# Kernel optimization log

Measured on AMD Instinct MI355X. Metric: run time of the kernel, lower is better.

The kernel has to match this reference:

```python
import jax, jax.numpy as jnp
import numpy as np

D = 256; H = 4; DK = 32; DV = D // H; DFF = 1024
NTF = 600; NG = 8000
EPS = 1e-5


def layer_norm(x, g, b):
    m = jnp.mean(x, -1, keepdims=True)
    v = jnp.mean((x - m) ** 2, -1, keepdims=True)
    return (x - m) / jnp.sqrt(v + EPS) * g + b


def setup_inputs() -> dict:
    key = jax.random.key(0)
    ks = jax.random.split(key, 32)
    def nrm(i, shape, s=1.0):
        return jax.random.normal(ks[i], shape, dtype=jnp.float32) * s
    w = 0.02  # init scale for weights
    inp = {
        "H_TF": nrm(0, (NTF, D)),
        "H_G": nrm(1, (NG, D)),
        "z_exp": nrm(2, (NG, D)),
        "z_seq": nrm(3, (NG, D)),
        "z_txt": nrm(4, (NG, D)),
        "tf_idx": jax.random.randint(ks[5], (NTF,), 0, NG),
        "WQ_seq": nrm(6, (H * DK, D), w), "WK_seq": nrm(7, (H * DK, D), w),
        "WQ_exp": nrm(8, (H * DK, D), w), "WK_exp": nrm(9, (H * DK, D), w),
        "WQ_txt": nrm(10, (H * DK, D), w), "WK_txt": nrm(11, (H * DK, D), w),
        "gate_w": jnp.broadcast_to(jnp.eye(3, dtype=jnp.float32), (H, 3, 3)),
        "gate_b": jnp.zeros((H, 3), jnp.float32),
        "WVG": nrm(12, (D, D), w), "WVTF": nrm(13, (D, D), w),
        "WOTF": nrm(14, (D, D), w), "WOG": nrm(15, (D, D), w),
        "ln_atf_g": jnp.ones((D,), jnp.float32), "ln_atf_b": jnp.zeros((D,), jnp.float32),
        "ln_ag_g": jnp.ones((D,), jnp.float32), "ln_ag_b": jnp.zeros((D,), jnp.float32),
        "ln_ftf_g": jnp.ones((D,), jnp.float32), "ln_ftf_b": jnp.zeros((D,), jnp.float32),
        "ln_fg_g": jnp.ones((D,), jnp.float32), "ln_fg_b": jnp.zeros((D,), jnp.float32),
        "ftf_W1": nrm(16, (DFF, D), w), "ftf_b1": jnp.zeros((DFF,), jnp.float32),
        "ftf_W2": nrm(17, (D, DFF), w), "ftf_b2": jnp.zeros((D,), jnp.float32),
        "fg_W1": nrm(18, (DFF, D), w), "fg_b1": jnp.zeros((DFF,), jnp.float32),
        "fg_W2": nrm(19, (D, DFF), w), "fg_b2": jnp.zeros((D,), jnp.float32),
    }
    return inp


def reference(H_TF, H_G, z_exp, z_seq, z_txt, tf_idx,
              WQ_seq, WK_seq, WQ_exp, WK_exp, WQ_txt, WK_txt,
              gate_w, gate_b, WVG, WVTF, WOTF, WOG,
              ln_atf_g, ln_atf_b, ln_ag_g, ln_ag_b,
              ln_ftf_g, ln_ftf_b, ln_fg_g, ln_fg_b,
              ftf_W1, ftf_b1, ftf_W2, ftf_b2,
              fg_W1, fg_b1, fg_W2, fg_b2):
    n_tf, n_gene = H_TF.shape[0], H_G.shape[0]
    scale = float(DK) ** 0.5

    H_TF_n = layer_norm(H_TF, ln_atf_g, ln_atf_b)
    H_G_n = layer_norm(H_G, ln_ag_g, ln_ag_b)

    z_seq_tf = z_seq[tf_idx]; z_exp_tf = z_exp[tf_idx]; z_txt_tf = z_txt[tf_idx]
    Q_seq = (z_seq_tf @ WQ_seq.T).reshape(n_tf, H, DK)
    K_seq = (z_seq @ WK_seq.T).reshape(n_gene, H, DK)
    Q_exp = (z_exp_tf @ WQ_exp.T).reshape(n_tf, H, DK)
    K_exp = (z_exp @ WK_exp.T).reshape(n_gene, H, DK)
    Q_txt = (z_txt_tf @ WQ_txt.T).reshape(n_tf, H, DK)
    K_txt = (z_txt @ WK_txt.T).reshape(n_gene, H, DK)

    s_bind = jnp.einsum('thd,ghd->htg', Q_seq, K_seq) / scale
    s_coexpr = jnp.einsum('thd,ghd->htg', Q_exp, K_exp) / scale
    s_know = jnp.einsum('thd,ghd->htg', Q_txt, K_txt) / scale

    # evidence gate: per-(head,tf,gene) softmax mixture over the 3 evidence channels
    s = jnp.stack([s_bind, s_coexpr, s_know], axis=-1)            # [H, t, g, 3]
    logits = jnp.einsum('htge,hef->htgf', s, gate_w) + gate_b[:, None, None, :]
    alpha = jax.nn.softmax(logits, axis=-1)                        # [H, t, g, 3]
    u = jnp.einsum('htge,htge->htg', alpha, s)                     # gated mixture
    A = jax.nn.softmax(u, axis=-1)                                 # softmax over genes

    V_G = (H_G_n @ WVG.T).reshape(n_gene, H, DV)
    V_TF = (H_TF_n @ WVTF.T).reshape(n_tf, H, DV)
    out_tf = jnp.einsum('htg,ghv->thv', A, V_G).reshape(n_tf, D) @ WOTF.T
    out_g = jnp.einsum('htg,thv->ghv', A, V_TF).reshape(n_gene, D) @ WOG.T

    H_TF2 = H_TF + out_tf
    H_G2 = H_G + out_g

    x = layer_norm(H_TF2, ln_ftf_g, ln_ftf_b)
    H_TF3 = H_TF2 + jax.nn.gelu(x @ ftf_W1.T + ftf_b1, approximate=False) @ ftf_W2.T + ftf_b2
    y = layer_norm(H_G2, ln_fg_g, ln_fg_b)
    H_G3 = H_G2 + jax.nn.gelu(y @ fg_W1.T + fg_b1, approximate=False) @ fg_W2.T + fg_b2

    return (H_TF3, H_G3, A.mean(0), u.mean(0), alpha.mean(0))
```

## Files before the change

### kernel.cpp

```cpp
#include <hip/hip_runtime.h>
#include <hip/hip_bf16.h>

#define NTF 600
#define NG  8000
#define DD  256
#define HH  4
#define DKK 32
#define DVV 64
#define DFF 1024

typedef __attribute__((ext_vector_type(8))) short frag_ab;
typedef __attribute__((ext_vector_type(4))) float frag_cd;

__device__ __forceinline__ unsigned short f2bu(float f) {
    __hip_bfloat16 h = __float2bfloat16(f);
    return __builtin_bit_cast(unsigned short, h);
}
__device__ __forceinline__ short f2bs(float f) { return (short)f2bu(f); }

__global__ __launch_bounds__(256)
void cvt3_kernel(const float* __restrict__ a, const float* __restrict__ b, const float* __restrict__ c,
                 unsigned short* __restrict__ oa, unsigned short* __restrict__ ob,
                 unsigned short* __restrict__ oc, int n4) {
    for (int i = blockIdx.x * 256 + threadIdx.x; i < 3 * n4; i += gridDim.x * 256) {
        int sel = i / n4, j = i - sel * n4;
        const float* src = (sel == 0) ? a : (sel == 1) ? b : c;
        unsigned short* dst = (sel == 0) ? oa : (sel == 1) ? ob : oc;
        float4 v = ((const float4*)src)[j];
        ushort4 o = {f2bu(v.x), f2bu(v.y), f2bu(v.z), f2bu(v.w)};
        ((ushort4*)dst)[j] = o;
    }
}

__global__ __launch_bounds__(256)
void cvt_w_kernel(const float* s0, const float* s1, const float* s2, const float* s3,
                  const float* s4, const float* s5, const float* s6, const float* s7,
                  const float* s8, const float* s9, const float* s10, const float* s11,
                  const float* s12, unsigned short* __restrict__ dst) {
    const int y = blockIdx.y;
    const float* src; int off, n;
    switch (y) {
        case 0:  src = s0;  off = 0;       n = 32768;  break;
        case 1:  src = s1;  off = 32768;   n = 32768;  break;
        case 2:  src = s2;  off = 65536;   n = 32768;  break;
        case 3:  src = s3;  off = 98304;   n = 32768;  break;
        case 4:  src = s4;  off = 131072;  n = 32768;  break;
        case 5:  src = s5;  off = 163840;  n = 32768;  break;
        case 6:  src = s6;  off = 196608;  n = 65536;  break;
        case 7:  src = s7;  off = 262144;  n = 65536;  break;
        case 8:  src = s8;  off = 327680;  n = 65536;  break;
        case 9:  src = s9;  off = 393216;  n = 262144; break;
        case 10: src = s10; off = 655360;  n = 262144; break;
        case 11: src = s11; off = 917504;  n = 262144; break;
        default: src = s12; off = 1179648; n = 262144; break;
    }
    const int n4 = n >> 2;
    for (int i = blockIdx.x * 256 + threadIdx.x; i < n4; i += gridDim.x * 256) {
        float4 v = ((const float4*)src)[i];
        ushort4 o = {f2bu(v.x), f2bu(v.y), f2bu(v.z), f2bu(v.w)};
        ((ushort4*)(dst + off))[i] = o;
    }
}

__global__ __launch_bounds__(64)
void ln_b_kernel(const float* __restrict__ x, const float* __restrict__ g,
                 const float* __restrict__ b, unsigned short* __restrict__ y) {
    int row = blockIdx.x;
    int tid = threadIdx.x;
    const float4* xp = (const float4*)(x + (size_t)row * DD);
    float4 v = xp[tid];
    float s = v.x + v.y + v.z + v.w;
    #pragma unroll
    for (int off = 32; off > 0; off >>= 1) s += __shfl_xor(s, off, 64);
    float mean = s * (1.f / 256.f);
    float dx = v.x - mean, dy = v.y - mean, dz = v.z - mean, dw = v.w - mean;
    float q = dx*dx + dy*dy + dz*dz + dw*dw;
    #pragma unroll
    for (int off = 32; off > 0; off >>= 1) q += __shfl_xor(q, off, 64);
    float inv = rsqrtf(q * (1.f / 256.f) + 1e-5f);
    float4 gg = ((const float4*)g)[tid];
    float4 bb = ((const float4*)b)[tid];
    ushort4 o = {f2bu(dx * inv * gg.x + bb.x), f2bu(dy * inv * gg.y + bb.y),
                 f2bu(dz * inv * gg.z + bb.z), f2bu(dw * inv * gg.w + bb.w)};
    ((ushort4*)(y + (size_t)row * DD))[tid] = o;
}

__global__ __launch_bounds__(256)
void gather_b_kernel(const float* __restrict__ zs, const float* __restrict__ ze,
                     const float* __restrict__ zt, const int* __restrict__ idx,
                     unsigned short* __restrict__ os, unsigned short* __restrict__ oe,
                     unsigned short* __restrict__ ot) {
    int t = blockIdx.x, j = threadIdx.x;
    size_t src = (size_t)idx[t] * DD + j;
    size_t dst = (size_t)t * DD + j;
    os[dst] = f2bu(zs[src]);
    oe[dst] = f2bu(ze[src]);
    ot[dst] = f2bu(zt[src]);
}

template<bool XF32, bool BIAS, bool GELU, bool RES, bool OB16>
__device__ __forceinline__
void mgemm_core(const void* __restrict__ Xv, const unsigned short* __restrict__ W,
                const float* __restrict__ bias, const float* __restrict__ res,
                void* __restrict__ Yv, int M, int N, int K) {
    const int lane = threadIdx.x & 63, wv = threadIdx.x >> 6;
    const int wm = wv >> 1, wn = wv & 1;
    const int lr = lane & 15, lk = lane >> 4;
    const int m0 = blockIdx.x * 64, n0 = blockIdx.y * 128;
    frag_cd zz = {0.f, 0.f, 0.f, 0.f};
    frag_cd acc[2][4];
    #pragma unroll
    for (int mi = 0; mi < 2; ++mi)
        #pragma unroll
        for (int ni = 0; ni < 4; ++ni) acc[mi][ni] = zz;
    int arow[2], brow[4];
    #pragma unroll
    for (int mi = 0; mi < 2; ++mi) arow[mi] = min(m0 + wm * 32 + mi * 16 + lr, M - 1);
    #pragma unroll
    for (int ni = 0; ni < 4; ++ni) brow[ni] = n0 + wn * 64 + ni * 16 + lr;
    for (int k0 = 0; k0 < K; k0 += 32) {
        frag_ab af[2], bfr[4];
        #pragma unroll
        for (int mi = 0; mi < 2; ++mi) {
            if (XF32) {
                const float* xp = (const float*)Xv + (size_t)arow[mi] * K + k0 + lk * 8;
                float4 v0 = *(const float4*)xp;
                float4 v1 = *(const float4*)(xp + 4);
                frag_ab t;
                t[0] = f2bs(v0.x); t[1] = f2bs(v0.y); t[2] = f2bs(v0.z); t[3] = f2bs(v0.w);
                t[4] = f2bs(v1.x); t[5] = f2bs(v1.y); t[6] = f2bs(v1.z); t[7] = f2bs(v1.w);
                af[mi] = t;
            } else {
                af[mi] = *(const frag_ab*)((const unsigned short*)Xv + (size_t)arow[mi] * K + k0 + lk * 8);
            }
        }
        #pragma unroll
        for (int ni = 0; ni < 4; ++ni)
            bfr[ni] = *(const frag_ab*)(W + (size_t)brow[ni] * K + k0 + lk * 8);
        #pragma unroll
        for (int mi = 0; mi < 2; ++mi)
            #pragma unroll
            for (int ni = 0; ni < 4; ++ni)
                acc[mi][ni] = __builtin_amdgcn_mfma_f32_16x16x32_bf16(af[mi], bfr[ni], acc[mi][ni], 0, 0, 0);
    }
    #pragma unroll
    for (int ni = 0; ni < 4; ++ni) {
        const int n = brow[ni];
        const float bn = BIAS ? bias[n] : 0.f;
        #pragma unroll
        for (int mi = 0; mi < 2; ++mi) {
            #pragma unroll
            for (int r = 0; r < 4; ++r) {
                const int m = m0 + wm * 32 + mi * 16 + lk * 4 + r;
                if (m < M) {
                    float v = acc[mi][ni][r] + bn;
                    if (GELU) v = 0.5f * v * (1.f + erff(v * 0.70710678118654752f));
                    if (RES)  v += res[(size_t)m * N + n];
                    if (OB16) ((unsigned short*)Yv)[(size_t)m * N + n] = f2bu(v);
                    else      ((float*)Yv)[(size_t)m * N + n] = v;
                }
            }
        }
    }
}

template<bool XF32, bool BIAS, bool GELU, bool RES, bool OB16>
__global__ __launch_bounds__(256)
void mgemm_kernel(const void* __restrict__ X, const unsigned short* __restrict__ W,
                  const float* __restrict__ bias, const float* __restrict__ res,
                  void* __restrict__ Y, int M, int N, int K) {
    mgemm_core<XF32, BIAS, GELU, RES, OB16>(X, W, bias, res, Y, M, N, K);
}

__global__ __launch_bounds__(256)
void mgemm3_kernel(const unsigned short* X0, const unsigned short* W0, unsigned short* Y0,
                   const unsigned short* X1, const unsigned short* W1, unsigned short* Y1,
                   const unsigned short* X2, const unsigned short* W2, unsigned short* Y2,
                   int M, int N, int K) {
    const unsigned short* X = (blockIdx.z == 0) ? X0 : (blockIdx.z == 1) ? X1 : X2;
    const unsigned short* W = (blockIdx.z == 0) ? W0 : (blockIdx.z == 1) ? W1 : W2;
    unsigned short*       Y = (blockIdx.z == 0) ? Y0 : (blockIdx.z == 1) ? Y1 : Y2;
    mgemm_core<false, false, false, false, true>(X, W, nullptr, nullptr, Y, M, N, K);
}

__global__ __launch_bounds__(256)
void scores_mfma(const unsigned short* __restrict__ Qse, const unsigned short* __restrict__ Qex,
                 const unsigned short* __restrict__ Qtx,
                 const unsigned short* __restrict__ Kse, const unsigned short* __restrict__ Kex,
                 const unsigned short* __restrict__ Ktx,
                 const float* __restrict__ gw, const float* __restrict__ gb,
                 float* __restrict__ U, float* __restrict__ umean, float* __restrict__ amean) {
    const int lane = threadIdx.x & 63, wv = threadIdx.x >> 6;
    const int lr = lane & 15, lk = lane >> 4;
    const int t0 = blockIdx.x * 64 + wv * 16;
    const int g0 = blockIdx.y * 64;
    const int tq = min(t0 + lr, NTF - 1);
    frag_cd zz = {0.f, 0.f, 0.f, 0.f};

    frag_ab qf[3][4];
    #pragma unroll
    for (int h = 0; h < HH; ++h) {
        qf[0][h] = *(const frag_ab*)(Qse + (size_t)tq * 128 + h * DKK + lk * 8);
        qf[1][h] = *(const frag_ab*)(Qex + (size_t)tq * 128 + h * DKK + lk * 8);
        qf[2][h] = *(const frag_ab*)(Qtx + (size_t)tq * 128 + h * DKK + lk * 8);
    }
    float gwr[HH][3][3], gbr[HH][3];
    #pragma unroll
    for (int h = 0; h < HH; ++h) {
        #pragma unroll
        for (int e = 0; e < 3; ++e)
            #pragma unroll
            for (int f = 0; f < 3; ++f) gwr[h][e][f] = gw[h * 9 + e * 3 + f];
        #pragma unroll
        for (int f = 0; f < 3; ++f) gbr[h][f] = gb[h * 3 + f];
    }
    const float sc = 0.17677669529663687f;

    #pragma unroll
    for (int gi = 0; gi < 4; ++gi) {
        const int gg = g0 + gi * 16;
        const int gk = gg + lr;
        float us[4] = {0.f, 0.f, 0.f, 0.f};
        float a0s[4] = {0.f, 0.f, 0.f, 0.f};
        float a1s[4] = {0.f, 0.f, 0.f, 0.f};
        float a2s[4] = {0.f, 0.f, 0.f, 0.f};
        #pragma unroll
        for (int h = 0; h < HH; ++h) {
            frag_ab kf0 = *(const frag_ab*)(Kse + (size_t)gk * 128 + h * DKK + lk * 8);
            frag_ab kf1 = *(const frag_ab*)(Kex + (size_t)gk * 128 + h * DKK + lk * 8);
            frag_ab kf2 = *(const frag_ab*)(Ktx + (size_t)gk * 128 + h * DKK + lk * 8);
            frag_cd s0 = __builtin_amdgcn_mfma_f32_16x16x32_bf16(qf[0][h], kf0, zz, 0, 0, 0);
            frag_cd s1 = __builtin_amdgcn_mfma_f32_16x16x32_bf16(qf[1][h], kf1, zz, 0, 0, 0);
            frag_cd s2 = __builtin_amdgcn_mfma_f32_16x16x32_bf16(qf[2][h], kf2, zz, 0, 0, 0);
            #pragma unroll
            for (int r = 0; r < 4; ++r) {
                const int t = t0 + lk * 4 + r;
                float e0 = s0[r] * sc, e1 = s1[r] * sc, e2 = s2[r] * sc;
                float lg0 = e0 * gwr[h][0][0] + e1 * gwr[h][1][0] + e2 * gwr[h][2][0] + gbr[h][0];
                float lg1 = e0 * gwr[h][0][1] + e1 * gwr[h][1][1] + e2 * gwr[h][2][1] + gbr[h][1];
                float lg2 = e0 * gwr[h][0][2] + e1 * gwr[h][1][2] + e2 * gwr[h][2][2] + gbr[h][2];
                float mx = fmaxf(lg0, fmaxf(lg1, lg2));
                float x0 = __expf(lg0 - mx), x1 = __expf(lg1 - mx), x2 = __expf(lg2 - mx);
                float inv = 1.f / (x0 + x1 + x2);
                float a0 = x0 * inv, a1 = x1 * inv, a2 = x2 * inv;
                float u = a0 * e0 + a1 * e1 + a2 * e2;
                if (t < NTF) U[((size_t)h * NTF + t) * NG + gg + lr] = u;
                us[r] += u; a0s[r] += a0; a1s[r] += a1; a2s[r] += a2;
            }
        }
        #pragma unroll
        for (int r = 0; r < 4; ++r) {
            const int t = t0 + lk * 4 + r;
            if (t < NTF) {
                size_t p = (size_t)t * NG + gg + lr;
                umean[p] = us[r] * 0.25f;
                amean[p * 3 + 0] = a0s[r] * 0.25f;
                amean[p * 3 + 1] = a1s[r] * 0.25f;
                amean[p * 3 + 2] = a2s[r] * 0.25f;
            }
        }
    }
}

__global__ __launch_bounds__(512)
void softmax_amean_kernel(float* __restrict__ U, float* __restrict__ Am) {
    __shared__ float sred[8];
    const int t = blockIdx.x, tid = threadIdx.x;
    const int w = tid >> 6;
    float am[16] = {};
    for (int h = 0; h < HH; ++h) {
        float* p = U + ((size_t)h * NTF + t) * NG;
        float v[16];
        float mx = -1e30f;
        #pragma unroll
        for (int i = 0; i < 16; ++i) {
            int j = i * 512 + tid;
            v[i] = (j < NG) ? p[j] : -1e30f;
            mx = fmaxf(mx, v[i]);
        }
        #pragma unroll
        for (int off = 32; off > 0; off >>= 1) mx = fmaxf(mx, __shfl_xor(mx, off, 64));
        __syncthreads();
        if ((tid & 63) == 0) sred[w] = mx;
        __syncthreads();
        mx = sred[0];
        #pragma unroll
        for (int k = 1; k < 8; ++k) mx = fmaxf(mx, sred[k]);
        float sum = 0.f;
        #pragma unroll
        for (int i = 0; i < 16; ++i) {
            int j = i * 512 + tid;
            v[i] = (j < NG) ? __expf(v[i] - mx) : 0.f;
            sum += v[i];
        }
        #pragma unroll
        for (int off = 32; off > 0; off >>= 1) sum += __shfl_xor(sum, off, 64);
        __syncthreads();
        if ((tid & 63) == 0) sred[w] = sum;
        __syncthreads();
        float tot = 0.f;
        #pragma unroll
        for (int k = 0; k < 8; ++k) tot += sred[k];
        float inv = 1.f / tot;
        #pragma unroll
        for (int i = 0; i < 16; ++i) {
            int j = i * 512 + tid;
            float a = v[i] * inv;
            if (j < NG) p[j] = a;
            am[i] += a;
        }
    }
    #pragma unroll
    for (int i = 0; i < 16; ++i) {
        int j = i * 512 + tid;
        if (j < NG) Am[(size_t)t * NG + j] = am[i] * 0.25f;
    }
}

__global__ __launch_bounds__(256)
void attn_tf_kernel(const float* __restrict__ A, const float* __restrict__ VG,
                    float* __restrict__ AT) {
    __shared__ float As[16][68];
    __shared__ float Vs[16][68];
    const int tid = threadIdx.x;
    const int tx = tid & 15, ty = tid >> 4;
    const int m0 = blockIdx.x * 64;
    const int h  = blockIdx.y;
    const int g0 = blockIdx.z * 512;
    const float* Ah = A + (size_t)h * NTF * NG;
    float acc[4][4] = {};
    for (int kk = 0; kk < 512; kk += 16) {
        __syncthreads();
        #pragma unroll
        for (int j = 0; j < 4; ++j) {
            int idx = j * 256 + tid;
            int k = idx & 15, m = idx >> 4;
            int t = m0 + m, g = g0 + kk + k;
            As[k][m] = (t < NTF && g < NG) ? Ah[(size_t)t * NG + g] : 0.f;
            int v = idx & 63, k2 = idx >> 6;
            int g2 = g0 + kk + k2;
            Vs[k2][v] = (g2 < NG) ? VG[(size_t)g2 * DD + h * DVV + v] : 0.f;
        }
        __syncthreads();
        #pragma unroll
        for (int k = 0; k < 16; ++k) {
            float4 a4 = *(const float4*)&As[k][ty * 4];
            float4 b4 = *(const float4*)&Vs[k][tx * 4];
            float a[4] = {a4.x, a4.y, a4.z, a4.w};
            float b[4] = {b4.x, b4.y, b4.z, b4.w};
            #pragma unroll
            for (int i = 0; i < 4; ++i)
                #pragma unroll
                for (int j = 0; j < 4; ++j)
                    acc[i][j] += a[i] * b[j];
        }
    }
    #pragma unroll
    for (int i = 0; i < 4; ++i) {
        int t = m0 + ty * 4 + i;
        if (t >= NTF) continue;
        #pragma unroll
        for (int j = 0; j < 4; ++j)
            atomicAdd(&AT[(size_t)t * DD + h * DVV + tx * 4 + j], acc[i][j]);
    }
}

__global__ __launch_bounds__(256)
void attn_g_kernel(const float* __restrict__ A, const float* __restrict__ VTF,
                   unsigned short* __restrict__ ATb) {
    __shared__ float As[16][68];
    __shared__ float Vs[16][68];
    const int tid = threadIdx.x;
    const int tx = tid & 15, ty = tid >> 4;
    const int g0 = blockIdx.x * 64;
    const int h  = blockIdx.y;
    const float* Ah = A + (size_t)h * NTF * NG;
    float acc[4][4] = {};
    for (int t0 = 0; t0 < NTF; t0 += 16) {
        __syncthreads();
        #pragma unroll
        for (int j = 0; j < 4; ++j) {
            int idx = j * 256 + tid;
            int m = idx & 63, k = idx >> 6;
            int t = t0 + k;
            As[k][m] = (t < NTF) ? Ah[(size_t)t * NG + g0 + m] : 0.f;
            Vs[k][m] = (t < NTF) ? VTF[(size_t)t * DD + h * DVV + m] : 0.f;
        }
        __syncthreads();
        #pragma unroll
        for (int k = 0; k < 16; ++k) {
            float4 a4 = *(const float4*)&As[k][ty * 4];
            float4 b4 = *(const float4*)&Vs[k][tx * 4];
            float a[4] = {a4.x, a4.y, a4.z, a4.w};
            float b[4] = {b4.x, b4.y, b4.z, b4.w};
            #pragma unroll
            for (int i = 0; i < 4; ++i)
                #pragma unroll
                for (int j = 0; j < 4; ++j)
                    acc[i][j] += a[i] * b[j];
        }
    }
    #pragma unroll
    for (int i = 0; i < 4; ++i) {
        ushort4 o = {f2bu(acc[i][0]), f2bu(acc[i][1]), f2bu(acc[i][2]), f2bu(acc[i][3])};
        *(ushort4*)&ATb[(size_t)(g0 + ty * 4 + i) * DD + h * DVV + tx * 4] = o;
    }
}

template<bool RES>
__global__ __launch_bounds__(256)
void gemm_xwt(const float* __restrict__ X, const float* __restrict__ W,
              const float* __restrict__ res, float* __restrict__ Y, int M, int N, int K) {
    __shared__ float Xs[16][132];
    __shared__ float Ws[16][132];
    const int tid = threadIdx.x;
    const int bm = blockIdx.x * 128, bn = blockIdx.y * 128;
    const int tx = tid & 15, ty = tid >> 4;
    float acc[8][8] = {};
    for (int k0 = 0; k0 < K; k0 += 16) {
        __syncthreads();
        #pragma unroll
        for (int j = 0; j < 8; ++j) {
            int idx = j * 256 + tid;
            int k = idx & 15, m = idx >> 4;
            Xs[k][m] = (bm + m < M) ? X[(size_t)(bm + m) * K + k0 + k] : 0.f;
            Ws[k][m] = W[(size_t)(bn + m) * K + k0 + k];
        }
        __syncthreads();
        #pragma unroll
        for (int k = 0; k < 16; ++k) {
            float4 a0 = *(const float4*)&Xs[k][ty * 8];
            float4 a1 = *(const float4*)&Xs[k][ty * 8 + 4];
            float4 b0 = *(const float4*)&Ws[k][tx * 8];
            float4 b1 = *(const float4*)&Ws[k][tx * 8 + 4];
            float a[8] = {a0.x,a0.y,a0.z,a0.w,a1.x,a1.y,a1.z,a1.w};
            float b[8] = {b0.x,b0.y,b0.z,b0.w,b1.x,b1.y,b1.z,b1.w};
            #pragma unroll
            for (int i = 0; i < 8; ++i)
                #pragma unroll
                for (int j = 0; j < 8; ++j)
                    acc[i][j] += a[i] * b[j];
        }
    }
    #pragma unroll
    for (int i = 0; i < 8; ++i) {
        int m = bm + ty * 8 + i;
        if (m >= M) continue;
        #pragma unroll
        for (int j = 0; j < 8; ++j) {
            int n = bn + tx * 8 + j;
            float v = acc[i][j];
            if (RES) v += res[(size_t)m * N + n];
            Y[(size_t)m * N + n] = v;
        }
    }
}

extern "C" void kernel_launch(void* const* d_in, const int* in_sizes, int n_in,
                              void* d_out, int out_size, void* d_ws, size_t ws_size,
                              hipStream_t stream) {
    (void)in_sizes; (void)n_in; (void)out_size; (void)ws_size;
    const float* H_TF   = (const float*)d_in[0];
    const float* H_G    = (const float*)d_in[1];
    const float* z_exp  = (const float*)d_in[2];
    const float* z_seq  = (const float*)d_in[3];
    const float* z_txt  = (const float*)d_in[4];
    const int*   tf_idx = (const int*)d_in[5];
    const float* WQ_seq = (const float*)d_in[6];
    const float* WK_seq = (const float*)d_in[7];
    const float* WQ_exp = (const float*)d_in[8];
    const float* WK_exp = (const float*)d_in[9];
    const float* WQ_txt = (const float*)d_in[10];
    const float* WK_txt = (const float*)d_in[11];
    const float* gate_w = (const float*)d_in[12];
    const float* gate_b = (const float*)d_in[13];
    const float* WVG    = (const float*)d_in[14];
    const float* WVTF   = (const float*)d_in[15];
    const float* WOTF   = (const float*)d_in[16];
    const float* WOG    = (const float*)d_in[17];
    const float* ln_atf_g = (const float*)d_in[18];
    const float* ln_atf_b = (const float*)d_in[19];
    const float* ln_ag_g  = (const float*)d_in[20];
    const float* ln_ag_b  = (const float*)d_in[21];
    const float* ln_ftf_g = (const float*)d_in[22];
    const float* ln_ftf_b = (const float*)d_in[23];
    const float* ln_fg_g  = (const float*)d_in[24];
    const float* ln_fg_b  = (const float*)d_in[25];
    const float* ftf_W1 = (const float*)d_in[26];
    const float* ftf_b1 = (const float*)d_in[27];
    const float* ftf_W2 = (const float*)d_in[28];
    const float* ftf_b2 = (const float*)d_in[29];
    const float* fg_W1  = (const float*)d_in[30];
    const float* fg_b1  = (const float*)d_in[31];
    const float* fg_W2  = (const float*)d_in[32];
    const float* fg_b2  = (const float*)d_in[33];

    float* out = (float*)d_out;
    float* out_HTF3  = out;
    float* out_HG3   = out + 153600;
    float* out_Amean = out + 2201600;
    float* out_umean = out + 7001600;
    float* out_amean = out + 11801600;

    float* ws = (float*)d_ws;
    float* U    = ws;
    float* VG   = ws + 19200000;
    float* VTF  = VG + 2048000;
    float* ATtf = VTF + 153600;
    float* HTF2 = ATtf + 153600;
    float* HG2  = HTF2 + 153600;
    float* G2 = U;
    float* G1 = U + 8192000;
    unsigned short* bws   = (unsigned short*)(ws + 23756800);
    unsigned short* Kb_se = bws;
    unsigned short* Kb_ex = bws + 1024000;
    unsigned short* Kb_tx = bws + 2048000;
    unsigned short* Qb_se = bws + 3072000;
    unsigned short* Qb_ex = bws + 3148800;
    unsigned short* Qb_tx = bws + 3225600;
    unsigned short* Wb    = bws + 3302400;
    unsigned short* HTFnb = bws + 4744192;
    unsigned short* HGnb  = bws + 4897792;
    unsigned short* zb_se = (unsigned short*)U;
    unsigned short* zb_ex = zb_se + 2048000;
    unsigned short* zb_tx = zb_se + 4096000;
    unsigned short* ztb_se = zb_se + 6144000;
    unsigned short* ztb_ex = ztb_se + 153600;
    unsigned short* ztb_tx = ztb_se + 307200;
    unsigned short* ATgb = (unsigned short*)VG;

    unsigned short* WQse_b = Wb + 0;
    unsigned short* WQex_b = Wb + 32768;
    unsigned short* WQtx_b = Wb + 65536;
    unsigned short* WKse_b = Wb + 98304;
    unsigned short* WKex_b = Wb + 131072;
    unsigned short* WKtx_b = Wb + 163840;
    unsigned short* WVGb   = Wb + 196608;
    unsigned short* WVTFb  = Wb + 262144;
    unsigned short* WOGb   = Wb + 327680;
    unsigned short* ftfW1b = Wb + 393216;
    unsigned short* ftfW2b = Wb + 655360;
    unsigned short* fgW1b  = Wb + 917504;
    unsigned short* fgW2b  = Wb + 1179648;

    cvt3_kernel<<<750, 256, 0, stream>>>(z_seq, z_exp, z_txt, zb_se, zb_ex, zb_tx, 512000);
    cvt_w_kernel<<<dim3(64, 13), 256, 0, stream>>>(
        WQ_seq, WQ_exp, WQ_txt, WK_seq, WK_exp, WK_txt,
        WVG, WVTF, WOG, ftf_W1, ftf_W2, fg_W1, fg_W2, Wb);

    ln_b_kernel<<<NTF, 64, 0, stream>>>(H_TF, ln_atf_g, ln_atf_b, HTFnb);
    ln_b_kernel<<<NG,  64, 0, stream>>>(H_G,  ln_ag_g,  ln_ag_b,  HGnb);

    gather_b_kernel<<<NTF, 256, 0, stream>>>(z_seq, z_exp, z_txt, tf_idx, ztb_se, ztb_ex, ztb_tx);

    mgemm3_kernel<<<dim3(10, 1, 3), 256, 0, stream>>>(ztb_se, WQse_b, Qb_se,
                                                      ztb_ex, WQex_b, Qb_ex,
                                                      ztb_tx, WQtx_b, Qb_tx, NTF, 128, DD);
    mgemm3_kernel<<<dim3(125, 1, 3), 256, 0, stream>>>(zb_se, WKse_b, Kb_se,
                                                       zb_ex, WKex_b, Kb_ex,
                                                       zb_tx, WKtx_b, Kb_tx, NG, 128, DD);
    mgemm_kernel<false,false,false,false,false><<<dim3(125, 2), 256, 0, stream>>>(
        HGnb, WVGb, nullptr, nullptr, VG, NG, DD, DD);
    mgemm_kernel<false,false,false,false,false><<<dim3(10, 2), 256, 0, stream>>>(
        HTFnb, WVTFb, nullptr, nullptr, VTF, NTF, DD, DD);

    scores_mfma<<<dim3(10, 125), 256, 0, stream>>>(
        Qb_se, Qb_ex, Qb_tx, Kb_se, Kb_ex, Kb_tx, gate_w, gate_b, U, out_umean, out_amean);

    softmax_amean_kernel<<<NTF, 512, 0, stream>>>(U, out_Amean);

    hipMemsetAsync(ATtf, 0, (size_t)NTF * DD * sizeof(float), stream);
    attn_tf_kernel<<<dim3(10, HH, 16), 256, 0, stream>>>(U, VG, ATtf);
    attn_g_kernel<<<dim3(NG / 64, HH), 256, 0, stream>>>(U, VTF, ATgb);

    gemm_xwt<true><<<dim3(5, 2), 256, 0, stream>>>(ATtf, WOTF, H_TF, HTF2, NTF, DD, DD);
    mgemm_kernel<false,false,false,true,false><<<dim3(125, 2), 256, 0, stream>>>(
        ATgb, WOGb, nullptr, H_G, HG2, NG, DD, DD);

    ln_b_kernel<<<NTF, 64, 0, stream>>>(HTF2, ln_ftf_g, ln_ftf_b, HTFnb);
    mgemm_kernel<false,true,true,false,false><<<dim3(10, 8), 256, 0, stream>>>(
        HTFnb, ftfW1b, ftf_b1, nullptr, G1, NTF, DFF, DD);
    mgemm_kernel<true,true,false,true,false><<<dim3(10, 2), 256, 0, stream>>>(
        G1, ftfW2b, ftf_b2, HTF2, out_HTF3, NTF, DD, DFF);

    ln_b_kernel<<<NG, 64, 0, stream>>>(HG2, ln_fg_g, ln_fg_b, HGnb);
    mgemm_kernel<false,true,true,false,false><<<dim3(125, 8), 256, 0, stream>>>(
        HGnb, fgW1b, fg_b1, nullptr, G2, NG, DFF, DD);
    mgemm_kernel<true,true,false,true,false><<<dim3(125, 2), 256, 0, stream>>>(
        G2, fgW2b, fg_b2, HG2, out_HG3, NG, DD, DFF);
}
```

Measured before the change: 730.9 us.

## Use bf16 MFMA for TF attention-value product with transposed bf16 V_G

Adds a kernel that transposes V_G per head into a bf16 [H*64, NG] layout, then replaces the fp32 shared-memory FMA GEMM for A·V_G with an MFMA 16x16x32 bf16 kernel. This kernel reads A rows straight from global memory and converts them to bf16 on the fly. The aim is to cut the ALU cost of the 600x8000x64 per-head product and drop the shared-memory staging. The trade-off is an extra transpose pass and lower precision for A and V, while split-K atomics remain.

Result: faster. 658.4 us (-9.9%).

```diff
diff --git a/kernel.cpp b/kernel.cpp
--- a/kernel.cpp
+++ b/kernel.cpp
@@ -318,50 +318,56 @@
 }
 
 __global__ __launch_bounds__(256)
-void attn_tf_kernel(const float* __restrict__ A, const float* __restrict__ VG,
-                    float* __restrict__ AT) {
-    __shared__ float As[16][68];
-    __shared__ float Vs[16][68];
+void vgt_kernel(const float* __restrict__ VG, unsigned short* __restrict__ VGT) {
+    __shared__ float tile[64][65];
+    const int g0 = blockIdx.x * 64;
+    const int h  = blockIdx.y;
     const int tid = threadIdx.x;
-    const int tx = tid & 15, ty = tid >> 4;
-    const int m0 = blockIdx.x * 64;
+    const int c = tid & 63, r0 = (tid >> 6) * 16;
+    #pragma unroll
+    for (int i = 0; i < 16; ++i)
+        tile[r0 + i][c] = VG[(size_t)(g0 + r0 + i) * DD + h * DVV + c];
+    __syncthreads();
+    #pragma unroll
+    for (int i = 0; i < 16; ++i)
+        VGT[(size_t)(h * 64 + r0 + i) * NG + g0 + c] = f2bu(tile[c][r0 + i]);
+}
+
+__global__ __launch_bounds__(256)
+void attn_tf_mfma(const float* __restrict__ A, const unsigned short* __restrict__ VGT,
+                  float* __restrict__ AT) {
+    const int lane = threadIdx.x & 63, wv = threadIdx.x >> 6;
+    const int lr = lane & 15, lk = lane >> 4;
+    const int t0 = blockIdx.x * 64 + wv * 16;
     const int h  = blockIdx.y;
-    const int g0 = blockIdx.z * 512;
-    const float* Ah = A + (size_t)h * NTF * NG;
-    float acc[4][4] = {};
-    for (int kk = 0; kk < 512; kk += 16) {
-        __syncthreads();
-        #pragma unroll
-        for (int j = 0; j < 4; ++j) {
-            int idx = j * 256 + tid;
-            int k = idx & 15, m = idx >> 4;
-            int t = m0 + m, g = g0 + kk + k;
-            As[k][m] = (t < NTF && g < NG) ? Ah[(size_t)t * NG + g] : 0.f;
-            int v = idx & 63, k2 = idx >> 6;
-            int g2 = g0 + kk + k2;
-            Vs[k2][v] = (g2 < NG) ? VG[(size_t)g2 * DD + h * DVV + v] : 0.f;
-        }
-        __syncthreads();
-        #pragma unroll
-        for (int k = 0; k < 16; ++k) {
-            float4 a4 = *(const float4*)&As[k][ty * 4];
-            float4 b4 = *(const float4*)&Vs[k][tx * 4];
-            float a[4] = {a4.x, a4.y, a4.z, a4.w};
-            float b[4] = {b4.x, b4.y, b4.z, b4.w};
-            #pragma unroll
-            for (int i = 0; i < 4; ++i)
-                #pragma unroll
-                for (int j = 0; j < 4; ++j)
-                    acc[i][j] += a[i] * b[j];
-        }
-    }
-    #pragma unroll
-    for (int i = 0; i < 4; ++i) {
-        int t = m0 + ty * 4 + i;
-        if (t >= NTF) continue;
-        #pragma unroll
-        for (int j = 0; j < 4; ++j)
-            atomicAdd(&AT[(size_t)t * DD + h * DVV + tx * 4 + j], acc[i][j]);
+    const int kbase = blockIdx.z * 512;
+    const float* arow = A + (size_t)h * NTF * NG + (size_t)min(t0 + lr, NTF - 1) * NG;
+    const unsigned short* Vh = VGT + (size_t)h * 64 * NG;
+    frag_cd zz = {0.f, 0.f, 0.f, 0.f};
+    frag_cd acc[4] = {zz, zz, zz, zz};
+    const int kend = min(kbase + 512, NG);
+    for (int k0 = kbase; k0 < kend; k0 += 32) {
+        const float* ap = arow + k0 + lk * 8;
+        float4 v0 = *(const float4*)ap;
+        float4 v1 = *(const float4*)(ap + 4);
+        frag_ab af;
+        af[0] = f2bs(v0.x); af[1] = f2bs(v0.y); af[2] = f2bs(v0.z); af[3] = f2bs(v0.w);
+        af[4] = f2bs(v1.x); af[5] = f2bs(v1.y); af[6] = f2bs(v1.z); af[7] = f2bs(v1.w);
+        #pragma unroll
+        for (int ni = 0; ni < 4; ++ni) {
+            frag_ab bf = *(const frag_ab*)(Vh + (size_t)(ni * 16 + lr) * NG + k0 + lk * 8);
+            acc[ni] = __builtin_amdgcn_mfma_f32_16x16x32_bf16(af, bf, acc[ni], 0, 0, 0);
+        }
+    }
+    #pragma unroll
+    for (int ni = 0; ni < 4; ++ni) {
+        const int v = ni * 16 + lr;
+        #pragma unroll
+        for (int r = 0; r < 4; ++r) {
+            const int t = t0 + lk * 4 + r;
+            if (t < NTF)
+                atomicAdd(&AT[(size_t)t * DD + h * DVV + v], acc[ni][r]);
+        }
     }
 }
 
@@ -521,6 +527,7 @@
     unsigned short* Wb    = bws + 3302400;
     unsigned short* HTFnb = bws + 4744192;
     unsigned short* HGnb  = bws + 4897792;
+    unsigned short* VGT   = bws + 6945792;
     unsigned short* zb_se = (unsigned short*)U;
     unsigned short* zb_ex = zb_se + 2048000;
     unsigned short* zb_tx = zb_se + 4096000;
@@ -564,13 +571,15 @@
     mgemm_kernel<false,false,false,false,false><<<dim3(10, 2), 256, 0, stream>>>(
         HTFnb, WVTFb, nullptr, nullptr, VTF, NTF, DD, DD);
 
+    vgt_kernel<<<dim3(125, HH), 256, 0, stream>>>(VG, VGT);
+
     scores_mfma<<<dim3(10, 125), 256, 0, stream>>>(
         Qb_se, Qb_ex, Qb_tx, Kb_se, Kb_ex, Kb_tx, gate_w, gate_b, U, out_umean, out_amean);
 
     softmax_amean_kernel<<<NTF, 512, 0, stream>>>(U, out_Amean);
 
     hipMemsetAsync(ATtf, 0, (size_t)NTF * DD * sizeof(float), stream);
-    attn_tf_kernel<<<dim3(10, HH, 16), 256, 0, stream>>>(U, VG, ATtf);
+    attn_tf_mfma<<<dim3(10, HH, 16), 256, 0, stream>>>(U, VGT, ATtf);
     attn_g_kernel<<<dim3(NG / 64, HH), 256, 0, stream>>>(U, VTF, ATgb);
 
     gemm_xwt<true><<<dim3(5, 2), 256, 0, stream>>>(ATtf, WOTF, H_TF, HTF2, NTF, DD, DD);
```
